# Optimization experiments

Measured on AMD Instinct MI355X. Metric: run time of the kernel, lower is better.

The kernel has to match this reference:

```python
import jax, jax.numpy as jnp
import numpy as np

MIN_FP16 = float(np.finfo(np.float16).min)  # -65504.0, matches torch.finfo(torch.float16).min


def _apply_rotary(x, cos, sin):
    # x: [B, H, S, D]; cos/sin: [S, D//2]
    # Equivalent to view_as_complex on interleaved pairs, multiply by freq_cis, view_as_real.
    xr = x[..., 0::2]
    xi = x[..., 1::2]
    c = cos[None, None]  # [1,1,S,D//2]
    s = sin[None, None]
    out_r = xr * c - xi * s
    out_i = xr * s + xi * c
    return jnp.stack([out_r, out_i], axis=-1).reshape(x.shape)


def setup_inputs() -> dict:
    key = jax.random.key(0)
    ks = jax.random.split(key, 4)
    B, S, D_MODEL, H = 2, 2048, 1024, 16
    HS = D_MODEL // H  # 64
    x = jax.random.normal(ks[0], (B, S, D_MODEL), dtype=jnp.float32)
    # Standard RoPE frequencies: theta_i = 10000^(-2i/HS)
    inv_freq = 1.0 / (10000.0 ** (np.arange(0, HS, 2, dtype=np.float32) / HS))  # [HS//2]
    t = np.arange(S, dtype=np.float32)
    angles = np.outer(t, inv_freq)  # [S, HS//2]
    cos = jnp.asarray(np.cos(angles))
    sin = jnp.asarray(np.sin(angles))
    mask = jnp.tril(jnp.ones((S, S), dtype=jnp.int32))[None, None]  # [1,1,S,S] causal
    scale = 1.0 / np.sqrt(D_MODEL)
    W_proj = jax.random.normal(ks[1], (D_MODEL, 3 * D_MODEL), dtype=jnp.float32) * scale
    b_proj = jnp.zeros((3 * D_MODEL,), dtype=jnp.float32)
    W_ff = jax.random.normal(ks[2], (D_MODEL, D_MODEL), dtype=jnp.float32) * scale
    b_ff = jnp.zeros((D_MODEL,), dtype=jnp.float32)
    return {"x": x, "cos_q": cos, "sin_q": sin, "cos_k": cos, "sin_k": sin,
            "mask": mask, "W_proj": W_proj, "b_proj": b_proj, "W_ff": W_ff, "b_ff": b_ff}


def reference(x, cos_q, sin_q, cos_k, sin_k, mask, W_proj, b_proj, W_ff, b_ff):
    B, S, d_model = x.shape
    H = 16
    HS = d_model // H
    head_scale = jnp.sqrt(jnp.float32(HS))

    # fused QKV projection, then split: [B,S,3*dm] -> [3,B,H,S,HS]
    x_proj = x @ W_proj + b_proj
    x_proj = x_proj.reshape(B, S, 3, H, HS).transpose(2, 0, 3, 1, 4)
    q, k, v = x_proj[0], x_proj[1], x_proj[2]

    # mask path: cache pre-RoPE k,v
    next_prefix_kv = jnp.stack([k, v])  # [2,B,H,S,HS]

    q = _apply_rotary(q, cos_q, sin_q)
    k = _apply_rotary(k, cos_k, sin_k)

    scores = jnp.einsum('bhqd,bhkd->bhqk', q, k) / head_scale
    scores = jnp.where(mask == 0, jnp.float32(MIN_FP16), scores)
    probs = jax.nn.softmax(scores, axis=-1)
    attn_o = jnp.einsum('bhqk,bhkd->bhqd', probs, v)  # [B,H,S,HS]

    attn_o = attn_o.transpose(0, 2, 1, 3).reshape(B, S, d_model)
    ff_o = attn_o @ W_ff + b_ff
    return ff_o, next_prefix_kv
```

## Files before the change

### kernel.cpp

```cpp
#include <hip/hip_runtime.h>
#include <stdint.h>

#define DM    1024
#define NH    16
#define HS    64
#define S_LEN 2048

typedef short bf16x8 __attribute__((ext_vector_type(8)));
typedef float f32x4  __attribute__((ext_vector_type(4)));
typedef unsigned short u16x4 __attribute__((ext_vector_type(4)));

__device__ __forceinline__ uint16_t f2b(float f) {
    union { float f; uint32_t i; } x; x.f = f;
    uint32_t r = x.i + 0x7fffu + ((x.i >> 16) & 1u);
    return (uint16_t)(r >> 16);
}
__device__ __forceinline__ uint32_t pack2(float a, float b) {
    return (uint32_t)f2b(a) | ((uint32_t)f2b(b) << 16);
}
__device__ __forceinline__ f32x4 mfma16(bf16x8 a, bf16x8 b, f32x4 c) {
    return __builtin_amdgcn_mfma_f32_16x16x32_bf16(a, b, c, 0, 0, 0);
}
__device__ __forceinline__ float fast_exp2(float x) {
    return __builtin_amdgcn_exp2f(x);
}
template<int CTRL>
__device__ __forceinline__ float dpp_max(float x) {
    union { float f; int i; } u; u.f = x;
    int y = __builtin_amdgcn_update_dpp(u.i, u.i, CTRL, 0xF, 0xF, true);
    union { int i; float f; } v; v.i = y;
    return fmaxf(x, v.f);
}

__global__ __launch_bounds__(256) void convert_bf16(
    const float* __restrict__ in, uint16_t* __restrict__ out)
{
    const size_t i = (size_t)blockIdx.x * 256 + threadIdx.x;
    const float4* p = (const float4*)in + i * 2;
    float4 a = p[0], b = p[1];
    uint4 o;
    o.x = pack2(a.x, a.y); o.y = pack2(a.z, a.w);
    o.z = pack2(b.x, b.y); o.w = pack2(b.z, b.w);
    ((uint4*)out)[i] = o;
}

__global__ __launch_bounds__(256) void transpose_w(
    const float* __restrict__ W, uint16_t* __restrict__ WT, int N)
{
    __shared__ float T[32][33];
    const int tx = threadIdx.x & 31, ty = threadIdx.x >> 5;
    const int n0 = blockIdx.x * 32, k0 = blockIdx.y * 32;
    #pragma unroll
    for (int i = 0; i < 4; ++i)
        T[ty + i * 8][tx] = W[(size_t)(k0 + ty + i * 8) * N + n0 + tx];
    __syncthreads();
    #pragma unroll
    for (int i = 0; i < 4; ++i)
        WT[(size_t)(n0 + ty + i * 8) * 1024 + k0 + tx] = f2b(T[tx][ty + i * 8]);
}

#define LOADK(K0, A_, B_)                                                                  \
    do {                                                                                   \
        if (ABF) {                                                                         \
            const uint16_t* ap_ = (const uint16_t*)Araw + (size_t)(m0 + sm) * 1024 + (K0) + skc; \
            A_ = *(const uint4*)ap_;                                                       \
        } else {                                                                           \
            const float* ap_ = (const float*)Araw + (size_t)(m0 + sm) * 1024 + (K0) + skc; \
            float4 f0_ = *(const float4*)(ap_ + 0),  f1_ = *(const float4*)(ap_ + 4);      \
            A_.x = pack2(f0_.x, f0_.y); A_.y = pack2(f0_.z, f0_.w);                        \
            A_.z = pack2(f1_.x, f1_.y); A_.w = pack2(f1_.z, f1_.w);                        \
        }                                                                                  \
        const uint16_t* bp_ = BT + (size_t)(n0 + sm) * 1024 + (K0) + skc;                  \
        B_ = *(const uint4*)bp_;                                                           \
    } while (0)

#define STOREK(BUF, A_, B_)                                                                \
    do {                                                                                   \
        *(uint4*)&As[BUF][sm][skc] = A_;                                                   \
        *(uint4*)&Bs[BUF][sm][skc] = B_;                                                   \
    } while (0)

#define COMPUTEK(BUF)                                                                      \
    do {                                                                                   \
        bf16x8 af_[2], bf_[4];                                                             \
        _Pragma("unroll")                                                                  \
        for (int mi = 0; mi < 2; ++mi)                                                     \
            af_[mi] = *(const bf16x8*)&As[BUF][wm + mi * 16 + li][quad * 8];               \
        _Pragma("unroll")                                                                  \
        for (int ni = 0; ni < 4; ++ni)                                                     \
            bf_[ni] = *(const bf16x8*)&Bs[BUF][wn + ni * 16 + li][quad * 8];               \
        _Pragma("unroll")                                                                  \
        for (int mi = 0; mi < 2; ++mi)                                                     \
            _Pragma("unroll")                                                              \
            for (int ni = 0; ni < 4; ++ni)                                                 \
                acc[mi][ni] = mfma16(af_[mi], bf_[ni], acc[mi][ni]);                       \
    } while (0)

#define STAGE_GLL(BUF, K0)                                                                 \
    do {                                                                                   \
        const uint16_t* ga_ = (const uint16_t*)Araw +                                      \
            (size_t)(m0 + wave * 16 + (lane >> 2)) * 1024 + (K0) + (lane & 3) * 8;         \
        __builtin_amdgcn_global_load_lds(                                                  \
            (const __attribute__((address_space(1))) void*)ga_,                            \
            (__attribute__((address_space(3))) void*)&As[BUF][wave * 16][0], 16, 0, 0);    \
        const uint16_t* gb_ = BT +                                                         \
            (size_t)(n0 + wave * 16 + (lane >> 2)) * 1024 + (K0) + (lane & 3) * 8;         \
        __builtin_amdgcn_global_load_lds(                                                  \
            (const __attribute__((address_space(1))) void*)gb_,                            \
            (__attribute__((address_space(3))) void*)&Bs[BUF][wave * 16][0], 16, 0, 0);    \
    } while (0)

template<int MODE, bool ABF, bool WV>
__global__ __launch_bounds__(512) void gemm_mfma(
    const void* __restrict__ Araw,
    const uint16_t* __restrict__ BT,
    const float* __restrict__ bias,
    int N,
    const float* __restrict__ cq, const float* __restrict__ sq,
    const float* __restrict__ ck, const float* __restrict__ sk,
    uint16_t* __restrict__ qbuf, uint16_t* __restrict__ kbuf,
    float* __restrict__ kout, float* __restrict__ vout,
    uint16_t* __restrict__ vtb,
    float* __restrict__ Cout)
{
    __shared__ uint16_t As[2][128][32];
    __shared__ uint16_t Bs[2][128][32];

    const int tid  = threadIdx.x;
    const int wave = tid >> 6, lane = tid & 63;
    const int quad = lane >> 4, li = lane & 15;
    const int wm = (wave >> 1) * 32, wn = (wave & 1) * 64;
    const int m0 = blockIdx.y * 128, n0 = blockIdx.x * 128;

    f32x4 acc[2][4];
    #pragma unroll
    for (int a = 0; a < 2; ++a)
        #pragma unroll
        for (int c = 0; c < 4; ++c)
            acc[a][c] = (f32x4){0.f, 0.f, 0.f, 0.f};

    const int sm = tid >> 2, skc = (tid & 3) * 8;

    if constexpr (ABF) {
        STAGE_GLL(0, 0);
        __syncthreads();
        for (int t = 0; t < 32; t += 2) {
            if (t + 1 < 32) STAGE_GLL(1, (t + 1) * 32);
            COMPUTEK(0);
            __syncthreads();
            if (t + 2 < 32) STAGE_GLL(0, (t + 2) * 32);
            COMPUTEK(1);
            __syncthreads();
        }
    } else {
        uint4 Aa, Ba, Ab, Bb;
        LOADK(0, Aa, Ba);
        STOREK(0, Aa, Ba);
        LOADK(32, Ab, Bb);
        __syncthreads();
        for (int t = 0; t < 16; ++t) {
            const int kb = t * 64;
            if (t < 15) LOADK(kb + 64, Aa, Ba);
            COMPUTEK(0);
            STOREK(1, Ab, Bb);
            __syncthreads();
            if (t < 15) LOADK(kb + 96, Ab, Bb);
            COMPUTEK(1);
            if (t < 15) {
                STOREK(0, Aa, Ba);
                __syncthreads();
            }
        }
    }

    if (MODE == 1) {
        #pragma unroll
        for (int ni = 0; ni < 4; ++ni) {
            const int n = n0 + wn + ni * 16 + li;
            const float bb = bias[n];
            #pragma unroll
            for (int mi = 0; mi < 2; ++mi)
                #pragma unroll
                for (int r = 0; r < 4; ++r) {
                    const int m = m0 + wm + mi * 16 + quad * 4 + r;
                    Cout[(size_t)m * N + n] = acc[mi][ni][r] + bb;
                }
        }
    } else {
        #pragma unroll
        for (int ni = 0; ni < 4; ++ni) {
            const int n   = n0 + wn + ni * 16 + li;
            const int sel = n >> 10;
            const int d   = n & 1023;
            const int h   = d >> 6;
            const int hd  = d & 63;
            const int i0  = hd >> 1;
            const float bb = bias[n];
            #pragma unroll
            for (int mi = 0; mi < 2; ++mi) {
                const int mb = m0 + wm + mi * 16 + quad * 4;
                const int b  = mb >> 11;
                const int s0 = mb & 2047;
                float vv[4];
                #pragma unroll
                for (int r = 0; r < 4; ++r) {
                    const int s = s0 + r;
                    const float val  = acc[mi][ni][r] + bb;
                    const float part = __shfl_xor(val, 1);
                    const size_t idx = ((size_t)(b * NH + h) * S_LEN + s) * HS + hd;
                    if (sel == 0) {
                        float c = cq[s * 32 + i0], sn = sq[s * 32 + i0];
                        float o = (hd & 1) ? (part * sn + val * c) : (val * c - part * sn);
                        qbuf[idx] = f2b(o * 0.18033688f);
                    } else if (sel == 1) {
                        kout[idx] = val;
                        float c = ck[s * 32 + i0], sn = sk[s * 32 + i0];
                        float o = (hd & 1) ? (part * sn + val * c) : (val * c - part * sn);
                        kbuf[idx] = f2b(o);
                    } else {
                        vout[idx] = val;
                        vv[r] = val;
                    }
                }
                if (WV && sel == 2) {
                    u16x4 u;
                    u[0] = f2b(vv[0]); u[1] = f2b(vv[1]);
                    u[2] = f2b(vv[2]); u[3] = f2b(vv[3]);
                    *(u16x4*)&vtb[((size_t)(b * NH + h) * HS + hd) * S_LEN + s0] = u;
                }
            }
        }
    }
}

__global__ __launch_bounds__(256) void attn_mfma(
    const uint16_t* __restrict__ qbuf,
    const uint16_t* __restrict__ kbuf,
    const uint16_t* __restrict__ vtb,
    uint16_t* __restrict__ obuf)
{
    __shared__ uint16_t Ks[64][72];
    __shared__ uint16_t Vt[64][72];
    __shared__ uint16_t Ps[64][68];

    const int i  = blockIdx.x;
    const int bh = i >> 5;
    const int jj = i & 31;
    const int g  = jj >> 3, cc = jj & 7;
    const int qt = (g == 0) ? (31 - cc) : (g == 1) ? cc : (g == 2) ? (23 - cc) : (8 + cc);
    const int h = bh & 15, b = bh >> 4;
    const int tid = threadIdx.x;
    const int wave = tid >> 6, lane = tid & 63;
    const int quad = lane >> 4, li = lane & 15;
    const int wrow0 = wave * 16;

    const short onebf = (short)0x3F80;
    const bf16x8 kOnes = {onebf, onebf, onebf, onebf, onebf, onebf, onebf, onebf};

    const uint16_t* qp = qbuf + ((size_t)bh * S_LEN + qt * 64 + wrow0 + li) * HS + quad * 8;
    const bf16x8 aq0 = *(const bf16x8*)qp;
    const bf16x8 aq1 = *(const bf16x8*)(qp + 32);

    f32x4 oacc[4];
    float m_i[4], l_i[4];
    #pragma unroll
    for (int r = 0; r < 4; ++r) {
        m_i[r] = -1e30f; l_i[r] = 0.f;
        oacc[r] = (f32x4){0.f, 0.f, 0.f, 0.f};
    }

    const int row = tid >> 2, c = (tid & 3) * 16;
    uint4 kr0, kr1, vr0, vr1;

    auto load_kv = [&](int kt) {
        const uint16_t* kp = kbuf + ((size_t)bh * S_LEN + kt * 64 + row) * HS + c;
        kr0 = *(const uint4*)kp;
        kr1 = *(const uint4*)(kp + 8);
        const uint16_t* vp = vtb + ((size_t)bh * HS + row) * S_LEN + kt * 64 + c;
        vr0 = *(const uint4*)vp;
        vr1 = *(const uint4*)(vp + 8);
    };
    load_kv(0);

    for (int kt = 0; kt <= qt; ++kt) {
        __syncthreads();
        *(uint4*)&Ks[row][c]     = kr0;
        *(uint4*)&Ks[row][c + 8] = kr1;
        *(uint4*)&Vt[row][c]     = vr0;
        *(uint4*)&Vt[row][c + 8] = vr1;
        __syncthreads();
        if (kt < qt) load_kv(kt + 1);

        f32x4 sacc[4];
        __builtin_amdgcn_s_setprio(1);
        #pragma unroll
        for (int ni = 0; ni < 4; ++ni) {
            bf16x8 b0 = *(const bf16x8*)&Ks[ni * 16 + li][quad * 8];
            bf16x8 b1 = *(const bf16x8*)&Ks[ni * 16 + li][32 + quad * 8];
            f32x4 z = (f32x4){0.f, 0.f, 0.f, 0.f};
            z = mfma16(aq0, b0, z);
            sacc[ni] = mfma16(aq1, b1, z);
        }
        __builtin_amdgcn_s_setprio(0);

        const bool diag = (kt == qt);
        float p[4][4];
        #pragma unroll
        for (int ni = 0; ni < 4; ++ni)
            #pragma unroll
            for (int r = 0; r < 4; ++r) {
                float v = sacc[ni][r];
                if (diag && (ni * 16 + li > wrow0 + quad * 4 + r)) v = -65504.f;
                p[ni][r] = v;
            }
        float alp[4];
        #pragma unroll
        for (int r = 0; r < 4; ++r) {
            float mx = fmaxf(fmaxf(p[0][r], p[1][r]), fmaxf(p[2][r], p[3][r]));
            mx = dpp_max<0xB1>(mx);
            mx = dpp_max<0x4E>(mx);
            mx = dpp_max<0x124>(mx);
            mx = dpp_max<0x128>(mx);
            float mnew  = fmaxf(m_i[r], mx);
            alp[r] = fast_exp2(m_i[r] - mnew);
            m_i[r] = mnew;
            #pragma unroll
            for (int ni = 0; ni < 4; ++ni)
                p[ni][r] = fast_exp2(p[ni][r] - mnew);
            #pragma unroll
            for (int ni = 0; ni < 4; ++ni) oacc[ni][r] *= alp[r];
        }

        #pragma unroll
        for (int ni = 0; ni < 4; ++ni)
            #pragma unroll
            for (int r = 0; r < 4; ++r)
                Ps[wrow0 + quad * 4 + r][ni * 16 + li] = f2b(p[ni][r]);

        bf16x8 pa0 = *(const bf16x8*)&Ps[wrow0 + li][quad * 8];
        bf16x8 pa1 = *(const bf16x8*)&Ps[wrow0 + li][32 + quad * 8];

        __builtin_amdgcn_s_setprio(1);
        f32x4 ls = (f32x4){0.f, 0.f, 0.f, 0.f};
        ls = mfma16(pa0, kOnes, ls);
        ls = mfma16(pa1, kOnes, ls);

        #pragma unroll
        for (int ni = 0; ni < 4; ++ni) {
            bf16x8 v0 = *(const bf16x8*)&Vt[ni * 16 + li][quad * 8];
            bf16x8 v1 = *(const bf16x8*)&Vt[ni * 16 + li][32 + quad * 8];
            oacc[ni] = mfma16(pa0, v0, oacc[ni]);
            oacc[ni] = mfma16(pa1, v1, oacc[ni]);
        }
        __builtin_amdgcn_s_setprio(0);

        #pragma unroll
        for (int r = 0; r < 4; ++r)
            l_i[r] = l_i[r] * alp[r] + ls[r];
    }

    #pragma unroll
    for (int ni = 0; ni < 4; ++ni)
        #pragma unroll
        for (int r = 0; r < 4; ++r) {
            const int qg = qt * 64 + wrow0 + quad * 4 + r;
            obuf[((size_t)b * S_LEN + qg) * DM + h * HS + ni * 16 + li] =
                f2b(oacc[ni][r] / l_i[r]);
        }
}

extern "C" void kernel_launch(void* const* d_in, const int* in_sizes, int n_in,
                              void* d_out, int out_size, void* d_ws, size_t ws_size,
                              hipStream_t stream) {
    const float* x  = (const float*)d_in[0];
    const float* cq = (const float*)d_in[1];
    const float* sq = (const float*)d_in[2];
    const float* ck = (const float*)d_in[3];
    const float* sk = (const float*)d_in[4];
    const float* Wp = (const float*)d_in[6];
    const float* bp = (const float*)d_in[7];
    const float* Wf = (const float*)d_in[8];
    const float* bf = (const float*)d_in[9];

    float* out  = (float*)d_out;
    float* ffo  = out;
    float* kout = out + 4194304;
    float* vout = out + 8388608;

    uint16_t* qbuf = (uint16_t*)d_ws;
    uint16_t* kbuf = qbuf + 4194304;
    uint16_t* abuf = kbuf + 4194304;
    uint16_t* vtb  = abuf + 4194304;
    uint16_t* xbf  = vtb  + 4194304;
    uint16_t* WpT  = abuf;
    uint16_t* WfT  = qbuf;

    const bool has_xbf = ws_size >= (size_t)40 * 1024 * 1024;

    dim3 blk(256), blkg(512);
    transpose_w<<<dim3(96, 32), blk, 0, stream>>>(Wp, WpT, 3072);
    if (has_xbf) {
        convert_bf16<<<dim3(2048), blk, 0, stream>>>(x, xbf);
        gemm_mfma<0, true, true><<<dim3(24, 32), blkg, 0, stream>>>(
            xbf, WpT, bp, 3072, cq, sq, ck, sk,
            qbuf, kbuf, kout, vout, vtb, nullptr);
    } else {
        gemm_mfma<0, false, true><<<dim3(24, 32), blkg, 0, stream>>>(
            x, WpT, bp, 3072, cq, sq, ck, sk,
            qbuf, kbuf, kout, vout, vtb, nullptr);
    }
    attn_mfma<<<dim3(1024), blk, 0, stream>>>(qbuf, kbuf, vtb, abuf);
    transpose_w<<<dim3(32, 32), blk, 0, stream>>>(Wf, WfT, 1024);
    gemm_mfma<1, true, false><<<dim3(8, 32), blkg, 0, stream>>>(
        abuf, WfT, bf, 1024, nullptr, nullptr, nullptr, nullptr,
        nullptr, nullptr, nullptr, nullptr, nullptr, ffo);
}
```

Measured before the change: 275.9 us.

## Pair causal query tiles per attention block and merge prep kernels

The attention kernel now gives each block two query tiles (pr and 31-pr), so every block does the same amount of causal work. This halves the grid to 512 blocks and prefetches the first K/V tile for the second pass. The weight transpose and the x-to-bf16 conversion are merged into one prep launch to save a kernel launch. The cost is less parallelism: 512 blocks on a 256-CU device, with a serial dependency between the two tiles inside each block.

```diff
diff --git a/kernel.cpp b/kernel.cpp
--- a/kernel.cpp
+++ b/kernel.cpp
@@ -32,24 +32,11 @@
     return fmaxf(x, v.f);
 }
 
-__global__ __launch_bounds__(256) void convert_bf16(
-    const float* __restrict__ in, uint16_t* __restrict__ out)
+__device__ __forceinline__ void transpose_tile(
+    const float* __restrict__ W, uint16_t* __restrict__ WT, int N,
+    int n0, int k0, float (*T)[33])
 {
-    const size_t i = (size_t)blockIdx.x * 256 + threadIdx.x;
-    const float4* p = (const float4*)in + i * 2;
-    float4 a = p[0], b = p[1];
-    uint4 o;
-    o.x = pack2(a.x, a.y); o.y = pack2(a.z, a.w);
-    o.z = pack2(b.x, b.y); o.w = pack2(b.z, b.w);
-    ((uint4*)out)[i] = o;
-}
-
-__global__ __launch_bounds__(256) void transpose_w(
-    const float* __restrict__ W, uint16_t* __restrict__ WT, int N)
-{
-    __shared__ float T[32][33];
     const int tx = threadIdx.x & 31, ty = threadIdx.x >> 5;
-    const int n0 = blockIdx.x * 32, k0 = blockIdx.y * 32;
     #pragma unroll
     for (int i = 0; i < 4; ++i)
         T[ty + i * 8][tx] = W[(size_t)(k0 + ty + i * 8) * N + n0 + tx];
@@ -57,6 +44,32 @@
     #pragma unroll
     for (int i = 0; i < 4; ++i)
         WT[(size_t)(n0 + ty + i * 8) * 1024 + k0 + tx] = f2b(T[tx][ty + i * 8]);
+}
+
+__global__ __launch_bounds__(256) void prep(
+    const float* __restrict__ x, uint16_t* __restrict__ xbf,
+    const float* __restrict__ Wp, uint16_t* __restrict__ WpT)
+{
+    __shared__ float T[32][33];
+    const int blk = blockIdx.x;
+    if (blk < 3072) {
+        transpose_tile(Wp, WpT, 3072, (blk % 96) * 32, (blk / 96) * 32, T);
+    } else {
+        const size_t i = (size_t)(blk - 3072) * 256 + threadIdx.x;
+        const float4* p = (const float4*)x + i * 2;
+        float4 a = p[0], b = p[1];
+        uint4 o;
+        o.x = pack2(a.x, a.y); o.y = pack2(a.z, a.w);
+        o.z = pack2(b.x, b.y); o.w = pack2(b.z, b.w);
+        ((uint4*)xbf)[i] = o;
+    }
+}
+
+__global__ __launch_bounds__(256) void transpose_w(
+    const float* __restrict__ W, uint16_t* __restrict__ WT, int N)
+{
+    __shared__ float T[32][33];
+    transpose_tile(W, WT, N, blockIdx.x * 32, blockIdx.y * 32, T);
 }
 
 #define LOADK(K0, A_, B_)                                                                  \
@@ -244,10 +257,8 @@
     __shared__ uint16_t Ps[64][68];
 
     const int i  = blockIdx.x;
-    const int bh = i >> 5;
-    const int jj = i & 31;
-    const int g  = jj >> 3, cc = jj & 7;
-    const int qt = (g == 0) ? (31 - cc) : (g == 1) ? cc : (g == 2) ? (23 - cc) : (8 + cc);
+    const int bh = i >> 4;
+    const int pr = i & 15;
     const int h = bh & 15, b = bh >> 4;
     const int tid = threadIdx.x;
     const int wave = tid >> 6, lane = tid & 63;
@@ -256,18 +267,6 @@
 
     const short onebf = (short)0x3F80;
     const bf16x8 kOnes = {onebf, onebf, onebf, onebf, onebf, onebf, onebf, onebf};
-
-    const uint16_t* qp = qbuf + ((size_t)bh * S_LEN + qt * 64 + wrow0 + li) * HS + quad * 8;
-    const bf16x8 aq0 = *(const bf16x8*)qp;
-    const bf16x8 aq1 = *(const bf16x8*)(qp + 32);
-
-    f32x4 oacc[4];
-    float m_i[4], l_i[4];
-    #pragma unroll
-    for (int r = 0; r < 4; ++r) {
-        m_i[r] = -1e30f; l_i[r] = 0.f;
-        oacc[r] = (f32x4){0.f, 0.f, 0.f, 0.f};
-    }
 
     const int row = tid >> 2, c = (tid & 3) * 16;
     uint4 kr0, kr1, vr0, vr1;
@@ -282,91 +281,108 @@
     };
     load_kv(0);
 
-    for (int kt = 0; kt <= qt; ++kt) {
-        __syncthreads();
-        *(uint4*)&Ks[row][c]     = kr0;
-        *(uint4*)&Ks[row][c + 8] = kr1;
-        *(uint4*)&Vt[row][c]     = vr0;
-        *(uint4*)&Vt[row][c + 8] = vr1;
-        __syncthreads();
-        if (kt < qt) load_kv(kt + 1);
-
-        f32x4 sacc[4];
-        __builtin_amdgcn_s_setprio(1);
+    for (int tt = 0; tt < 2; ++tt) {
+        const int qt = tt ? (31 - pr) : pr;
+
+        const uint16_t* qp = qbuf + ((size_t)bh * S_LEN + qt * 64 + wrow0 + li) * HS + quad * 8;
+        const bf16x8 aq0 = *(const bf16x8*)qp;
+        const bf16x8 aq1 = *(const bf16x8*)(qp + 32);
+
+        f32x4 oacc[4];
+        float m_i[4], l_i[4];
         #pragma unroll
-        for (int ni = 0; ni < 4; ++ni) {
-            bf16x8 b0 = *(const bf16x8*)&Ks[ni * 16 + li][quad * 8];
-            bf16x8 b1 = *(const bf16x8*)&Ks[ni * 16 + li][32 + quad * 8];
-            f32x4 z = (f32x4){0.f, 0.f, 0.f, 0.f};
-            z = mfma16(aq0, b0, z);
-            sacc[ni] = mfma16(aq1, b1, z);
-        }
-        __builtin_amdgcn_s_setprio(0);
-
-        const bool diag = (kt == qt);
-        float p[4][4];
+        for (int r = 0; r < 4; ++r) {
+            m_i[r] = -1e30f; l_i[r] = 0.f;
+            oacc[r] = (f32x4){0.f, 0.f, 0.f, 0.f};
+        }
+
+        for (int kt = 0; kt <= qt; ++kt) {
+            __syncthreads();
+            *(uint4*)&Ks[row][c]     = kr0;
+            *(uint4*)&Ks[row][c + 8] = kr1;
+            *(uint4*)&Vt[row][c]     = vr0;
+            *(uint4*)&Vt[row][c + 8] = vr1;
+            __syncthreads();
+            if (kt < qt)       load_kv(kt + 1);
+            else if (tt == 0)  load_kv(0);
+
+            f32x4 sacc[4];
+            __builtin_amdgcn_s_setprio(1);
+            #pragma unroll
+            for (int ni = 0; ni < 4; ++ni) {
+                bf16x8 b0 = *(const bf16x8*)&Ks[ni * 16 + li][quad * 8];
+                bf16x8 b1 = *(const bf16x8*)&Ks[ni * 16 + li][32 + quad * 8];
+                f32x4 z = (f32x4){0.f, 0.f, 0.f, 0.f};
+                z = mfma16(aq0, b0, z);
+                sacc[ni] = mfma16(aq1, b1, z);
+            }
+            __builtin_amdgcn_s_setprio(0);
+
+            const bool diag = (kt == qt);
+            float p[4][4];
+            #pragma unroll
+            for (int ni = 0; ni < 4; ++ni)
+                #pragma unroll
+                for (int r = 0; r < 4; ++r) {
+                    float v = sacc[ni][r];
+                    if (diag && (ni * 16 + li > wrow0 + quad * 4 + r)) v = -65504.f;
+                    p[ni][r] = v;
+                }
+            float alp[4];
+            #pragma unroll
+            for (int r = 0; r < 4; ++r) {
+                float mx = fmaxf(fmaxf(p[0][r], p[1][r]), fmaxf(p[2][r], p[3][r]));
+                mx = dpp_max<0xB1>(mx);
+                mx = dpp_max<0x4E>(mx);
+                mx = dpp_max<0x124>(mx);
+                mx = dpp_max<0x128>(mx);
+                float mnew  = fmaxf(m_i[r], mx);
+                alp[r] = fast_exp2(m_i[r] - mnew);
+                m_i[r] = mnew;
+                #pragma unroll
+                for (int ni = 0; ni < 4; ++ni)
+                    p[ni][r] = fast_exp2(p[ni][r] - mnew);
+                #pragma unroll
+                for (int ni = 0; ni < 4; ++ni) oacc[ni][r] *= alp[r];
+            }
+
+            #pragma unroll
+            for (int ni = 0; ni < 4; ++ni)
+                #pragma unroll
+                for (int r = 0; r < 4; ++r)
+                    Ps[wrow0 + quad * 4 + r][ni * 16 + li] = f2b(p[ni][r]);
+
+            bf16x8 pa0 = *(const bf16x8*)&Ps[wrow0 + li][quad * 8];
+            bf16x8 pa1 = *(const bf16x8*)&Ps[wrow0 + li][32 + quad * 8];
+
+            __builtin_amdgcn_s_setprio(1);
+            f32x4 ls = (f32x4){0.f, 0.f, 0.f, 0.f};
+            ls = mfma16(pa0, kOnes, ls);
+            ls = mfma16(pa1, kOnes, ls);
+
+            #pragma unroll
+            for (int ni = 0; ni < 4; ++ni) {
+                bf16x8 v0 = *(const bf16x8*)&Vt[ni * 16 + li][quad * 8];
+                bf16x8 v1 = *(const bf16x8*)&Vt[ni * 16 + li][32 + quad * 8];
+                oacc[ni] = mfma16(pa0, v0, oacc[ni]);
+                oacc[ni] = mfma16(pa1, v1, oacc[ni]);
+            }
+            __builtin_amdgcn_s_setprio(0);
+
+            #pragma unroll
+            for (int r = 0; r < 4; ++r)
+                l_i[r] = l_i[r] * alp[r] + ls[r];
+        }
+
         #pragma unroll
         for (int ni = 0; ni < 4; ++ni)
             #pragma unroll
             for (int r = 0; r < 4; ++r) {
-                float v = sacc[ni][r];
-                if (diag && (ni * 16 + li > wrow0 + quad * 4 + r)) v = -65504.f;
-                p[ni][r] = v;
-            }
-        float alp[4];
-        #pragma unroll
-        for (int r = 0; r < 4; ++r) {
-            float mx = fmaxf(fmaxf(p[0][r], p[1][r]), fmaxf(p[2][r], p[3][r]));
-            mx = dpp_max<0xB1>(mx);
-            mx = dpp_max<0x4E>(mx);
-            mx = dpp_max<0x124>(mx);
-            mx = dpp_max<0x128>(mx);
-            float mnew  = fmaxf(m_i[r], mx);
-            alp[r] = fast_exp2(m_i[r] - mnew);
-            m_i[r] = mnew;
-            #pragma unroll
-            for (int ni = 0; ni < 4; ++ni)
-                p[ni][r] = fast_exp2(p[ni][r] - mnew);
-            #pragma unroll
-            for (int ni = 0; ni < 4; ++ni) oacc[ni][r] *= alp[r];
-        }
-
-        #pragma unroll
-        for (int ni = 0; ni < 4; ++ni)
-            #pragma unroll
-            for (int r = 0; r < 4; ++r)
-                Ps[wrow0 + quad * 4 + r][ni * 16 + li] = f2b(p[ni][r]);
-
-        bf16x8 pa0 = *(const bf16x8*)&Ps[wrow0 + li][quad * 8];
-        bf16x8 pa1 = *(const bf16x8*)&Ps[wrow0 + li][32 + quad * 8];
-
-        __builtin_amdgcn_s_setprio(1);
-        f32x4 ls = (f32x4){0.f, 0.f, 0.f, 0.f};
-        ls = mfma16(pa0, kOnes, ls);
-        ls = mfma16(pa1, kOnes, ls);
-
-        #pragma unroll
-        for (int ni = 0; ni < 4; ++ni) {
-            bf16x8 v0 = *(const bf16x8*)&Vt[ni * 16 + li][quad * 8];
-            bf16x8 v1 = *(const bf16x8*)&Vt[ni * 16 + li][32 + quad * 8];
-            oacc[ni] = mfma16(pa0, v0, oacc[ni]);
-            oacc[ni] = mfma16(pa1, v1, oacc[ni]);
-        }
-        __builtin_amdgcn_s_setprio(0);
-
-        #pragma unroll
-        for (int r = 0; r < 4; ++r)
-            l_i[r] = l_i[r] * alp[r] + ls[r];
+                const int qg = qt * 64 + wrow0 + quad * 4 + r;
+                obuf[((size_t)b * S_LEN + qg) * DM + h * HS + ni * 16 + li] =
+                    f2b(oacc[ni][r] / l_i[r]);
+            }
     }
-
-    #pragma unroll
-    for (int ni = 0; ni < 4; ++ni)
-        #pragma unroll
-        for (int r = 0; r < 4; ++r) {
-            const int qg = qt * 64 + wrow0 + quad * 4 + r;
-            obuf[((size_t)b * S_LEN + qg) * DM + h * HS + ni * 16 + li] =
-                f2b(oacc[ni][r] / l_i[r]);
-        }
 }
 
 extern "C" void kernel_launch(void* const* d_in, const int* in_sizes, int n_in,
@@ -398,18 +414,18 @@
     const bool has_xbf = ws_size >= (size_t)40 * 1024 * 1024;
 
     dim3 blk(256), blkg(512);
-    transpose_w<<<dim3(96, 32), blk, 0, stream>>>(Wp, WpT, 3072);
     if (has_xbf) {
-        convert_bf16<<<dim3(2048), blk, 0, stream>>>(x, xbf);
+        prep<<<dim3(5120), blk, 0, stream>>>(x, xbf, Wp, WpT);
         gemm_mfma<0, true, true><<<dim3(24, 32), blkg, 0, stream>>>(
             xbf, WpT, bp, 3072, cq, sq, ck, sk,
             qbuf, kbuf, kout, vout, vtb, nullptr);
     } else {
+        transpose_w<<<dim3(96, 32), blk, 0, stream>>>(Wp, WpT, 3072);
         gemm_mfma<0, false, true><<<dim3(24, 32), blkg, 0, stream>>>(
             x, WpT, bp, 3072, cq, sq, ck, sk,
             qbuf, kbuf, kout, vout, vtb, nullptr);
     }
-    attn_mfma<<<dim3(1024), blk, 0, stream>>>(qbuf, kbuf, vtb, abuf);
+    attn_mfma<<<dim3(512), blk, 0, stream>>>(qbuf, kbuf, vtb, abuf);
     transpose_w<<<dim3(32, 32), blk, 0, stream>>>(Wf, WfT, 1024);
     gemm_mfma<1, true, false><<<dim3(8, 32), blkg, 0, stream>>>(
         abuf, WfT, bf, 1024, nullptr, nullptr, nullptr, nullptr,
```

Result: faster. 251.1 us (-9.0%).
